# Kernel optimization log

Measured on AMD Instinct MI355X. Metric: run time of the kernel, lower is better.

The kernel has to match this reference:

```python
import jax, jax.numpy as jnp
import numpy as np

NUM_HEADS = 16
HEIGHT = 32
WIDTH = 32
FEATURES_DIM = HEIGHT * WIDTH  # 1024
EMBED_DIM = 1024


def setup_inputs() -> dict:
    key = jax.random.key(0)
    ks = jax.random.split(key, 9)
    s_in = 1.0 / np.sqrt(FEATURES_DIM)
    s_e = 1.0 / np.sqrt(EMBED_DIM)
    return {
        "x": jax.random.normal(ks[0], (16, 512, HEIGHT, WIDTH), dtype=jnp.float32),
        "Wq": jax.random.uniform(ks[1], (EMBED_DIM, FEATURES_DIM), jnp.float32, -s_in, s_in),
        "bq": jax.random.uniform(ks[2], (EMBED_DIM,), jnp.float32, -s_in, s_in),
        "Wk": jax.random.uniform(ks[3], (EMBED_DIM, FEATURES_DIM), jnp.float32, -s_in, s_in),
        "bk": jax.random.uniform(ks[4], (EMBED_DIM,), jnp.float32, -s_in, s_in),
        "Wv": jax.random.uniform(ks[5], (EMBED_DIM, FEATURES_DIM), jnp.float32, -s_in, s_in),
        "bv": jax.random.uniform(ks[6], (EMBED_DIM,), jnp.float32, -s_in, s_in),
        "Wo": jax.random.uniform(ks[7], (FEATURES_DIM, EMBED_DIM), jnp.float32, -s_e, s_e),
        "bo": jax.random.uniform(ks[8], (FEATURES_DIM,), jnp.float32, -s_e, s_e),
    }


def reference(x, Wq, bq, Wk, bk, Wv, bv, Wo, bo):
    B, C, H, W = x.shape
    nh = NUM_HEADS
    hd = EMBED_DIM // nh
    xf = x.reshape(B, C, H * W)  # [B, C, F] - channel tokens
    q = xf @ Wq.T + bq  # [B, C, E]
    k = xf @ Wk.T + bk
    v = xf @ Wv.T + bv
    q = q.reshape(B, C, nh, hd).transpose(0, 2, 1, 3)  # [B, nh, C, hd]
    k = k.reshape(B, C, nh, hd).transpose(0, 2, 1, 3)
    v = v.reshape(B, C, nh, hd).transpose(0, 2, 1, 3)
    scores = jnp.einsum("bhcd,bhkd->bhck", q, k) / jnp.sqrt(jnp.float32(hd))
    attn = jax.nn.softmax(scores, axis=-1)
    out = jnp.einsum("bhck,bhkd->bhcd", attn, v)  # [B, nh, C, hd]
    out = out.transpose(0, 2, 1, 3).reshape(B, C, EMBED_DIM)
    out = out @ Wo.T + bo  # [B, C, F]
    return out.reshape(B, C, H, W)
```

## Files before the change

kernel.cpp:

```cpp
#include <hip/hip_runtime.h>


typedef unsigned short u16;
typedef __attribute__((ext_vector_type(8))) short short8;
typedef __attribute__((ext_vector_type(4))) float f32x4;
typedef __attribute__((ext_vector_type(16))) float f32x16;
typedef __attribute__((ext_vector_type(4))) unsigned short u16x4;

#define MFMA16(a, b, c) __builtin_amdgcn_mfma_f32_16x16x32_bf16(a, b, c, 0, 0, 0)
#define MFMA32(a, b, c) __builtin_amdgcn_mfma_f32_32x32x16_bf16(a, b, c, 0, 0, 0)

__device__ __forceinline__ u16 f2bf(float x) {
  unsigned u = __float_as_uint(x);
  u += 0x7FFFu + ((u >> 16) & 1u);
  return (u16)(u >> 16);
}

__device__ __forceinline__ void async16(const void* g, void* l) {
  __builtin_amdgcn_global_load_lds(
      (__attribute__((address_space(1))) unsigned int*)(g),
      (__attribute__((address_space(3))) unsigned int*)(l), 16, 0, 0);
}

__global__ __launch_bounds__(256) void cvt_all(
    const float* __restrict__ x, const float* __restrict__ wq,
    const float* __restrict__ wk, const float* __restrict__ wv,
    const float* __restrict__ wo, u16* __restrict__ dst) {
  int g = blockIdx.x * 256 + threadIdx.x;
  const float* s;
  int off;
  if (g < 2097152) {
    s = x; off = g;
  } else {
    int r = g - 2097152;
    int w = r >> 18;
    off = r & 262143;
    s = (w == 0) ? wq : (w == 1) ? wk : (w == 2) ? wv : wo;
  }
  f32x4 v = ((const f32x4*)s)[off];
  u16x4 o;
#pragma unroll
  for (int j = 0; j < 4; ++j) o[j] = f2bf(v[j]);
  ((u16x4*)dst)[g] = o;
}

__device__ __forceinline__ void gemm32(const u16* __restrict__ A,
                                       const u16* __restrict__ W,
                                       int m0, int n0, u16* lds,
                                       f32x16 acc[2][2]) {
  const int t = threadIdx.x;
  const int wave = t >> 6, lane = t & 63, r31 = lane & 31, l5 = lane >> 5;
  const int wr = wave >> 2, wn = wave & 3;
  const int srow = t >> 3;
  const int scol = ((t & 7) ^ ((t >> 3) & 7)) << 3;
  const u16* gA = A + (size_t)(m0 + srow) * 1024 + scol;
  const u16* gB = W + (size_t)(n0 + srow) * 1024 + scol;
  u16* stA = lds + wave * 512;
  u16* stB = lds + 8192 + wave * 512;
  const int xk = r31 & 7;
  const int arow = (wr * 64 + r31) * 64;
  const int brow = 8192 + (wn * 64 + r31) * 64;
  int soff[4];
#pragma unroll
  for (int ks = 0; ks < 4; ++ks) soff[ks] = ((ks * 2 + l5) ^ xk) << 3;

#define STAGEA(buf, k0)                                     \
  {                                                         \
    async16(gA + (k0), stA + (buf) * 24576);                \
    async16(gA + 65536 + (k0), stA + (buf) * 24576 + 4096); \
  }
#define STAGEB(buf, k0)                                                   \
  {                                                                       \
    async16(gB + (k0), stB + (buf) * 24576);                              \
    async16(gB + 65536 + (k0), stB + (buf) * 24576 + 4096);               \
    async16(gB + 131072 + (k0), stB + (buf) * 24576 + 8192);              \
    async16(gB + 196608 + (k0), stB + (buf) * 24576 + 12288);             \
  }

  STAGEA(0, 0); STAGEB(0, 0);
  STAGEA(1, 64); STAGEB(1, 64);
  asm volatile("s_waitcnt vmcnt(6)" ::: "memory");
  __builtin_amdgcn_s_barrier();

#pragma unroll
  for (int tt = 0; tt < 16; ++tt) {
    const u16* bufp = lds + (tt % 3) * 24576;
    short8 av[2][4], bv[2][4];
#pragma unroll
    for (int ks = 0; ks < 4; ++ks) {
      av[0][ks] = *(const short8*)(bufp + arow + soff[ks]);
      av[1][ks] = *(const short8*)(bufp + arow + 2048 + soff[ks]);
      bv[0][ks] = *(const short8*)(bufp + brow + soff[ks]);
      bv[1][ks] = *(const short8*)(bufp + brow + 2048 + soff[ks]);
    }
    if (tt < 14) {
      const int nb = (tt + 2) % 3, kn = (tt + 2) * 64;
      STAGEA(nb, kn); STAGEB(nb, kn);
    }
    __builtin_amdgcn_s_setprio(1);
#pragma unroll
    for (int ks = 0; ks < 4; ++ks)
#pragma unroll
      for (int mf = 0; mf < 2; ++mf)
#pragma unroll
        for (int nf = 0; nf < 2; ++nf)
          acc[mf][nf] = MFMA32(av[mf][ks], bv[nf][ks], acc[mf][nf]);
    __builtin_amdgcn_s_setprio(0);
    if (tt < 14) {
      asm volatile("s_waitcnt vmcnt(6)" ::: "memory");
    } else {
      asm volatile("s_waitcnt vmcnt(0)" ::: "memory");
    }
    __builtin_amdgcn_s_barrier();
  }
#undef STAGEA
#undef STAGEB
}

__global__ __launch_bounds__(512, 2) void gemm_qkv(
    const u16* __restrict__ xb, const u16* __restrict__ wq,
    const u16* __restrict__ wk, const u16* __restrict__ wv,
    const float* __restrict__ bq, const float* __restrict__ bk,
    const float* __restrict__ bv, u16* __restrict__ qo, u16* __restrict__ ko,
    u16* __restrict__ vo) {
  __shared__ u16 lds[73728];
  const int id = blockIdx.x;
  const int lid = (id & 7) * 96 + (id >> 3);
  const int z = lid >> 8;
  const int rem = lid & 255;
  const int m0 = (rem >> 2) * 128, n0 = (rem & 3) * 256;
  const u16* W = (z == 0) ? wq : (z == 1) ? wk : wv;
  const float* bias = (z == 0) ? bq : (z == 1) ? bk : bv;
  u16* outp = (z == 0) ? qo : (z == 1) ? ko : vo;
  f32x16 acc[2][2];
#pragma unroll
  for (int i = 0; i < 2; ++i)
#pragma unroll
    for (int j = 0; j < 2; ++j)
#pragma unroll
      for (int r = 0; r < 16; ++r) acc[i][j][r] = 0.f;
  gemm32(xb, W, m0, n0, lds, acc);

  const int t = threadIdx.x;
  const int wave = t >> 6, lane = t & 63, r31 = lane & 31, l5 = lane >> 5;
  const int wr = wave >> 2, wn = wave & 3;
  float bb[2];
#pragma unroll
  for (int nf = 0; nf < 2; ++nf) bb[nf] = bias[n0 + wn * 64 + nf * 32 + r31];
#pragma unroll
  for (int mf = 0; mf < 2; ++mf)
#pragma unroll
    for (int nf = 0; nf < 2; ++nf)
#pragma unroll
      for (int r = 0; r < 16; ++r) {
        int m = m0 + wr * 64 + mf * 32 + (r & 3) + ((r >> 2) << 3) + (l5 << 2);
        int n = n0 + wn * 64 + nf * 32 + r31;
        float val = acc[mf][nf][r] + bb[nf];
        int b_ = m >> 9, c = m & 511, h = n >> 6, dd = n & 63;
        int idx = (z == 2) ? ((((b_ << 4) + h) << 15) + (dd << 9) + c)
                           : ((((b_ << 4) + h) << 15) + (c << 6) + dd);
        outp[idx] = f2bf(val);
      }
}

__global__ __launch_bounds__(512, 2) void gemm_oproj(const u16* __restrict__ ab,
                                                     const u16* __restrict__ wo,
                                                     const float* __restrict__ bo,
                                                     float* __restrict__ out) {
  __shared__ u16 lds[73728];
  const int id = blockIdx.x;
  const int lid = (id & 7) * 32 + (id >> 3);
  const int m0 = (lid >> 2) * 128, n0 = (lid & 3) * 256;
  f32x16 acc[2][2];
#pragma unroll
  for (int i = 0; i < 2; ++i)
#pragma unroll
    for (int j = 0; j < 2; ++j)
#pragma unroll
      for (int r = 0; r < 16; ++r) acc[i][j][r] = 0.f;
  gemm32(ab, wo, m0, n0, lds, acc);

  const int t = threadIdx.x;
  const int wave = t >> 6, lane = t & 63, r31 = lane & 31, l5 = lane >> 5;
  const int wr = wave >> 2, wn = wave & 3;
  float bb[2];
#pragma unroll
  for (int nf = 0; nf < 2; ++nf) bb[nf] = bo[n0 + wn * 64 + nf * 32 + r31];
#pragma unroll
  for (int mf = 0; mf < 2; ++mf)
#pragma unroll
    for (int nf = 0; nf < 2; ++nf)
#pragma unroll
      for (int r = 0; r < 16; ++r) {
        int m = m0 + wr * 64 + mf * 32 + (r & 3) + ((r >> 2) << 3) + (l5 << 2);
        int n = n0 + wn * 64 + nf * 32 + r31;
        out[m * 1024 + n] = acc[mf][nf][r] + bb[nf];
      }
}

__global__ __launch_bounds__(512, 2) void attn_kernel(
    const u16* __restrict__ qb, const u16* __restrict__ kb,
    const u16* __restrict__ vb, u16* __restrict__ ab) {
  __shared__ u16 lK[32768];
  __shared__ u16 lV[32768];
  __shared__ u16 lP[8192];
  const int t = threadIdx.x;
  const int bh = blockIdx.x;
  const int b_ = bh >> 4, h_ = bh & 15;
  const u16* kg = kb + bh * 32768;
  const u16* vg = vb + bh * 32768;
#pragma unroll
  for (int i = 0; i < 8; ++i) {
    int row = i * 64 + (t >> 3), slot = t & 7;
    short8 kv = *(const short8*)(kg + row * 64 + slot * 8);
    *(short8*)(lK + row * 64 + ((slot ^ (row & 7)) << 3)) = kv;
    int vrow = i * 8 + (t >> 6), vslot = t & 63;
    short8 vv = *(const short8*)(vg + vrow * 512 + vslot * 8);
    *(short8*)(lV + vrow * 512 + ((vslot ^ (vrow & 7)) << 3)) = vv;
  }
  __syncthreads();

  const int wv_ = t >> 6, lane = t & 63, lr = lane & 15, lg = lane >> 4;
  u16* lPw = lP + wv_ * 1024;
  const u16* qg = qb + bh * 32768;
  const float sc = 0.125f * 1.44269504088896f;

#pragma unroll 1
  for (int qi = 0; qi < 4; ++qi) {
    const int qrow = (wv_ * 4 + qi) * 16;
    short8 a0 = *(const short8*)(qg + (qrow + lr) * 64 + lg * 8);
    short8 a1 = *(const short8*)(qg + (qrow + lr) * 64 + 32 + lg * 8);
    f32x4 s[32];
#pragma unroll
    for (int f = 0; f < 32; ++f) {
      const u16* kr = lK + (f * 16 + lr) * 64;
      short8 k0 = *(const short8*)(kr + ((lg ^ (lr & 7)) << 3));
      short8 k1 = *(const short8*)(kr + (((4 + lg) ^ (lr & 7)) << 3));
      f32x4 z4 = (f32x4){0.f, 0.f, 0.f, 0.f};
      z4 = MFMA16(a0, k0, z4);
      z4 = MFMA16(a1, k1, z4);
      s[f] = z4;
    }
    float inv[4];
#pragma unroll
    for (int r = 0; r < 4; ++r) {
      float m_ = s[0][r];
#pragma unroll
      for (int f = 1; f < 32; ++f) m_ = fmaxf(m_, s[f][r]);
      m_ = fmaxf(m_, __shfl_xor(m_, 1));
      m_ = fmaxf(m_, __shfl_xor(m_, 2));
      m_ = fmaxf(m_, __shfl_xor(m_, 4));
      m_ = fmaxf(m_, __shfl_xor(m_, 8));
      float sm = 0.f;
#pragma unroll
      for (int f = 0; f < 32; ++f) {
        float e = exp2f((s[f][r] - m_) * sc);
        s[f][r] = e;
        sm += e;
      }
      sm += __shfl_xor(sm, 1);
      sm += __shfl_xor(sm, 2);
      sm += __shfl_xor(sm, 4);
      sm += __shfl_xor(sm, 8);
      inv[r] = 1.f / sm;
    }
    f32x4 o[4];
#pragma unroll
    for (int i = 0; i < 4; ++i) o[i] = (f32x4){0.f, 0.f, 0.f, 0.f};
#pragma unroll
    for (int ch = 0; ch < 8; ++ch) {
#pragma unroll
      for (int cf = 0; cf < 4; ++cf)
#pragma unroll
        for (int r = 0; r < 4; ++r) {
          int q = lg * 4 + r, kc = cf * 16 + lr;
          lPw[q * 64 + (((kc >> 3) ^ (q & 7)) << 3) + (kc & 7)] =
              f2bf(s[ch * 4 + cf][r]);
        }
      asm volatile("s_waitcnt lgkmcnt(0)" ::: "memory");
      const u16* pr = lPw + lr * 64;
      short8 pa0 = *(const short8*)(pr + ((lg ^ (lr & 7)) << 3));
      short8 pa1 = *(const short8*)(pr + (((4 + lg) ^ (lr & 7)) << 3));
#pragma unroll
      for (int df = 0; df < 4; ++df) {
        const u16* vr = lV + (df * 16 + lr) * 512;
        short8 v0 = *(const short8*)(vr + (((ch * 8 + lg) ^ (lr & 7)) << 3));
        short8 v1 =
            *(const short8*)(vr + (((ch * 8 + 4 + lg) ^ (lr & 7)) << 3));
        o[df] = MFMA16(pa0, v0, o[df]);
        o[df] = MFMA16(pa1, v1, o[df]);
      }
    }
#pragma unroll
    for (int df = 0; df < 4; ++df)
#pragma unroll
      for (int r = 0; r < 4; ++r) {
        int q = qrow + lg * 4 + r, dd = df * 16 + lr;
        ab[(b_ * 512 + q) * 1024 + h_ * 64 + dd] = f2bf(o[df][r] * inv[r]);
      }
  }
}

extern "C" void kernel_launch(void* const* d_in, const int* in_sizes, int n_in,
                              void* d_out, int out_size, void* d_ws,
                              size_t ws_size, hipStream_t stream) {
  (void)in_sizes; (void)n_in; (void)out_size;
  const float* x  = (const float*)d_in[0];
  const float* Wq = (const float*)d_in[1];
  const float* bq = (const float*)d_in[2];
  const float* Wk = (const float*)d_in[3];
  const float* bk = (const float*)d_in[4];
  const float* Wv = (const float*)d_in[5];
  const float* bv = (const float*)d_in[6];
  const float* Wo = (const float*)d_in[7];
  const float* bo = (const float*)d_in[8];
  float* out = (float*)d_out;

  if (ws_size < 75497472u) return;
  u16* xb  = (u16*)d_ws;
  u16* wqb = xb + 8388608;
  u16* wkb = wqb + 1048576;
  u16* wvb = wkb + 1048576;
  u16* wob = wvb + 1048576;
  u16* qbuf = wob + 1048576;
  u16* kbuf = qbuf + 8388608;
  u16* vbuf = kbuf + 8388608;
  u16* abuf = xb;

  cvt_all<<<12288, 256, 0, stream>>>(x, Wq, Wk, Wv, Wo, xb);
  gemm_qkv<<<768, 512, 0, stream>>>(xb, wqb, wkb, wvb, bq, bk, bv,
                                    qbuf, kbuf, vbuf);
  attn_kernel<<<256, 512, 0, stream>>>(qbuf, kbuf, vbuf, abuf);
  gemm_oproj<<<256, 512, 0, stream>>>(abuf, wob, bo, out);
}
```

Before: 188.0 us.

## Switch shared GEMM core to 16x16x32 MFMA with two-phase interleaved loads

Replaces the 32x32x16 bf16 MFMA tiling in the QKV and output-projection GEMMs with a 4x4 grid of 16x16x32 MFMAs per wave, using new LDS swizzle offsets and a matching epilogue. Each 64-wide K step is split into two halves, and the global-to-LDS staging is split the same way so async loads interleave with the two MFMA bursts. Extra barriers and sched_barrier calls are added to enforce that ordering. This trades more barriers and smaller MFMA instructions for finer-grained overlap of loads and compute, and different register pressure.

Result: faster. 167.6 us (-10.9%).

```diff
diff --git a/kernel.cpp b/kernel.cpp
--- a/kernel.cpp
+++ b/kernel.cpp
@@ -4,11 +4,9 @@
 typedef unsigned short u16;
 typedef __attribute__((ext_vector_type(8))) short short8;
 typedef __attribute__((ext_vector_type(4))) float f32x4;
-typedef __attribute__((ext_vector_type(16))) float f32x16;
 typedef __attribute__((ext_vector_type(4))) unsigned short u16x4;
 
 #define MFMA16(a, b, c) __builtin_amdgcn_mfma_f32_16x16x32_bf16(a, b, c, 0, 0, 0)
-#define MFMA32(a, b, c) __builtin_amdgcn_mfma_f32_32x32x16_bf16(a, b, c, 0, 0, 0)
 
 __device__ __forceinline__ u16 f2bf(float x) {
   unsigned u = __float_as_uint(x);
@@ -44,12 +42,12 @@
   ((u16x4*)dst)[g] = o;
 }
 
-__device__ __forceinline__ void gemm32(const u16* __restrict__ A,
+__device__ __forceinline__ void gemm16(const u16* __restrict__ A,
                                        const u16* __restrict__ W,
                                        int m0, int n0, u16* lds,
-                                       f32x16 acc[2][2]) {
+                                       f32x4 acc[4][4]) {
   const int t = threadIdx.x;
-  const int wave = t >> 6, lane = t & 63, r31 = lane & 31, l5 = lane >> 5;
+  const int wave = t >> 6, lane = t & 63, lr = lane & 15, lg = lane >> 4;
   const int wr = wave >> 2, wn = wave & 3;
   const int srow = t >> 3;
   const int scol = ((t & 7) ^ ((t >> 3) & 7)) << 3;
@@ -57,54 +55,68 @@
   const u16* gB = W + (size_t)(n0 + srow) * 1024 + scol;
   u16* stA = lds + wave * 512;
   u16* stB = lds + 8192 + wave * 512;
-  const int xk = r31 & 7;
-  const int arow = (wr * 64 + r31) * 64;
-  const int brow = 8192 + (wn * 64 + r31) * 64;
-  int soff[4];
-#pragma unroll
-  for (int ks = 0; ks < 4; ++ks) soff[ks] = ((ks * 2 + l5) ^ xk) << 3;
+  const int aoff = (wr * 64 + lr) * 64;
+  const int boff = 8192 + (wn * 64 + lr) * 64;
+  const int sw0 = (lg ^ (lr & 7)) << 3;
+  const int sw1 = ((4 ^ lg) ^ (lr & 7)) << 3;
 
 #define STAGEA(buf, k0)                                     \
   {                                                         \
     async16(gA + (k0), stA + (buf) * 24576);                \
     async16(gA + 65536 + (k0), stA + (buf) * 24576 + 4096); \
   }
-#define STAGEB(buf, k0)                                                   \
-  {                                                                       \
-    async16(gB + (k0), stB + (buf) * 24576);                              \
-    async16(gB + 65536 + (k0), stB + (buf) * 24576 + 4096);               \
-    async16(gB + 131072 + (k0), stB + (buf) * 24576 + 8192);              \
-    async16(gB + 196608 + (k0), stB + (buf) * 24576 + 12288);             \
-  }
-
-  STAGEA(0, 0); STAGEB(0, 0);
-  STAGEA(1, 64); STAGEB(1, 64);
+#define STAGEB1(buf, k0) async16(gB + (k0), stB + (buf) * 24576);
+#define STAGEB3(buf, k0)                                       \
+  {                                                            \
+    async16(gB + 65536 + (k0), stB + (buf) * 24576 + 4096);    \
+    async16(gB + 131072 + (k0), stB + (buf) * 24576 + 8192);   \
+    async16(gB + 196608 + (k0), stB + (buf) * 24576 + 12288);  \
+  }
+
+  STAGEA(0, 0); STAGEB1(0, 0); STAGEB3(0, 0);
+  STAGEA(1, 64); STAGEB1(1, 64); STAGEB3(1, 64);
   asm volatile("s_waitcnt vmcnt(6)" ::: "memory");
   __builtin_amdgcn_s_barrier();
 
 #pragma unroll
   for (int tt = 0; tt < 16; ++tt) {
     const u16* bufp = lds + (tt % 3) * 24576;
-    short8 av[2][4], bv[2][4];
-#pragma unroll
-    for (int ks = 0; ks < 4; ++ks) {
-      av[0][ks] = *(const short8*)(bufp + arow + soff[ks]);
-      av[1][ks] = *(const short8*)(bufp + arow + 2048 + soff[ks]);
-      bv[0][ks] = *(const short8*)(bufp + brow + soff[ks]);
-      bv[1][ks] = *(const short8*)(bufp + brow + 2048 + soff[ks]);
-    }
-    if (tt < 14) {
-      const int nb = (tt + 2) % 3, kn = (tt + 2) * 64;
-      STAGEA(nb, kn); STAGEB(nb, kn);
-    }
+    const int nb = (tt + 2) % 3, kn = (tt + 2) * 64;
+    short8 av[4], bv[4];
+#pragma unroll
+    for (int m = 0; m < 4; ++m)
+      av[m] = *(const short8*)(bufp + aoff + m * 1024 + sw0);
+#pragma unroll
+    for (int n = 0; n < 4; ++n)
+      bv[n] = *(const short8*)(bufp + boff + n * 1024 + sw0);
+    if (tt < 14) { STAGEA(nb, kn); STAGEB1(nb, kn); }
+    __builtin_amdgcn_s_barrier();
+    asm volatile("s_waitcnt lgkmcnt(0)" ::: "memory");
+    __builtin_amdgcn_sched_barrier(0);
     __builtin_amdgcn_s_setprio(1);
 #pragma unroll
-    for (int ks = 0; ks < 4; ++ks)
-#pragma unroll
-      for (int mf = 0; mf < 2; ++mf)
-#pragma unroll
-        for (int nf = 0; nf < 2; ++nf)
-          acc[mf][nf] = MFMA32(av[mf][ks], bv[nf][ks], acc[mf][nf]);
+    for (int m = 0; m < 4; ++m)
+#pragma unroll
+      for (int n = 0; n < 4; ++n)
+        acc[m][n] = MFMA16(av[m], bv[n], acc[m][n]);
+    __builtin_amdgcn_s_setprio(0);
+    __builtin_amdgcn_s_barrier();
+#pragma unroll
+    for (int m = 0; m < 4; ++m)
+      av[m] = *(const short8*)(bufp + aoff + m * 1024 + sw1);
+#pragma unroll
+    for (int n = 0; n < 4; ++n)
+      bv[n] = *(const short8*)(bufp + boff + n * 1024 + sw1);
+    if (tt < 14) STAGEB3(nb, kn);
+    __builtin_amdgcn_s_barrier();
+    asm volatile("s_waitcnt lgkmcnt(0)" ::: "memory");
+    __builtin_amdgcn_sched_barrier(0);
+    __builtin_amdgcn_s_setprio(1);
+#pragma unroll
+    for (int m = 0; m < 4; ++m)
+#pragma unroll
+      for (int n = 0; n < 4; ++n)
+        acc[m][n] = MFMA16(av[m], bv[n], acc[m][n]);
     __builtin_amdgcn_s_setprio(0);
     if (tt < 14) {
       asm volatile("s_waitcnt vmcnt(6)" ::: "memory");
@@ -114,7 +126,8 @@
     __builtin_amdgcn_s_barrier();
   }
 #undef STAGEA
-#undef STAGEB
+#undef STAGEB1
+#undef STAGEB3
 }
 
 __global__ __launch_bounds__(512, 2) void gemm_qkv(
@@ -132,29 +145,27 @@
   const u16* W = (z == 0) ? wq : (z == 1) ? wk : wv;
   const float* bias = (z == 0) ? bq : (z == 1) ? bk : bv;
   u16* outp = (z == 0) ? qo : (z == 1) ? ko : vo;
-  f32x16 acc[2][2];
-#pragma unroll
-  for (int i = 0; i < 2; ++i)
-#pragma unroll
-    for (int j = 0; j < 2; ++j)
-#pragma unroll
-      for (int r = 0; r < 16; ++r) acc[i][j][r] = 0.f;
-  gemm32(xb, W, m0, n0, lds, acc);
+  f32x4 acc[4][4];
+#pragma unroll
+  for (int i = 0; i < 4; ++i)
+#pragma unroll
+    for (int j = 0; j < 4; ++j) acc[i][j] = (f32x4){0.f, 0.f, 0.f, 0.f};
+  gemm16(xb, W, m0, n0, lds, acc);
 
   const int t = threadIdx.x;
-  const int wave = t >> 6, lane = t & 63, r31 = lane & 31, l5 = lane >> 5;
+  const int wave = t >> 6, lane = t & 63, lr = lane & 15, lg = lane >> 4;
   const int wr = wave >> 2, wn = wave & 3;
-  float bb[2];
-#pragma unroll
-  for (int nf = 0; nf < 2; ++nf) bb[nf] = bias[n0 + wn * 64 + nf * 32 + r31];
-#pragma unroll
-  for (int mf = 0; mf < 2; ++mf)
-#pragma unroll
-    for (int nf = 0; nf < 2; ++nf)
-#pragma unroll
-      for (int r = 0; r < 16; ++r) {
-        int m = m0 + wr * 64 + mf * 32 + (r & 3) + ((r >> 2) << 3) + (l5 << 2);
-        int n = n0 + wn * 64 + nf * 32 + r31;
+  float bb[4];
+#pragma unroll
+  for (int nf = 0; nf < 4; ++nf) bb[nf] = bias[n0 + wn * 64 + nf * 16 + lr];
+#pragma unroll
+  for (int mf = 0; mf < 4; ++mf)
+#pragma unroll
+    for (int nf = 0; nf < 4; ++nf)
+#pragma unroll
+      for (int r = 0; r < 4; ++r) {
+        int m = m0 + wr * 64 + mf * 16 + lg * 4 + r;
+        int n = n0 + wn * 64 + nf * 16 + lr;
         float val = acc[mf][nf][r] + bb[nf];
         int b_ = m >> 9, c = m & 511, h = n >> 6, dd = n & 63;
         int idx = (z == 2) ? ((((b_ << 4) + h) << 15) + (dd << 9) + c)
@@ -171,29 +182,27 @@
   const int id = blockIdx.x;
   const int lid = (id & 7) * 32 + (id >> 3);
   const int m0 = (lid >> 2) * 128, n0 = (lid & 3) * 256;
-  f32x16 acc[2][2];
-#pragma unroll
-  for (int i = 0; i < 2; ++i)
-#pragma unroll
-    for (int j = 0; j < 2; ++j)
-#pragma unroll
-      for (int r = 0; r < 16; ++r) acc[i][j][r] = 0.f;
-  gemm32(ab, wo, m0, n0, lds, acc);
+  f32x4 acc[4][4];
+#pragma unroll
+  for (int i = 0; i < 4; ++i)
+#pragma unroll
+    for (int j = 0; j < 4; ++j) acc[i][j] = (f32x4){0.f, 0.f, 0.f, 0.f};
+  gemm16(ab, wo, m0, n0, lds, acc);
 
   const int t = threadIdx.x;
-  const int wave = t >> 6, lane = t & 63, r31 = lane & 31, l5 = lane >> 5;
+  const int wave = t >> 6, lane = t & 63, lr = lane & 15, lg = lane >> 4;
   const int wr = wave >> 2, wn = wave & 3;
-  float bb[2];
-#pragma unroll
-  for (int nf = 0; nf < 2; ++nf) bb[nf] = bo[n0 + wn * 64 + nf * 32 + r31];
-#pragma unroll
-  for (int mf = 0; mf < 2; ++mf)
-#pragma unroll
-    for (int nf = 0; nf < 2; ++nf)
-#pragma unroll
-      for (int r = 0; r < 16; ++r) {
-        int m = m0 + wr * 64 + mf * 32 + (r & 3) + ((r >> 2) << 3) + (l5 << 2);
-        int n = n0 + wn * 64 + nf * 32 + r31;
+  float bb[4];
+#pragma unroll
+  for (int nf = 0; nf < 4; ++nf) bb[nf] = bo[n0 + wn * 64 + nf * 16 + lr];
+#pragma unroll
+  for (int mf = 0; mf < 4; ++mf)
+#pragma unroll
+    for (int nf = 0; nf < 4; ++nf)
+#pragma unroll
+      for (int r = 0; r < 4; ++r) {
+        int m = m0 + wr * 64 + mf * 16 + lg * 4 + r;
+        int n = n0 + wn * 64 + nf * 16 + lr;
         out[m * 1024 + n] = acc[mf][nf][r] + bb[nf];
       }
 }
```
